# Optimization experiments

Hardware: AMD Instinct MI355X
Metric: run time of the kernel (lower is better)

The kernel has to match this reference:

```python
import jax, jax.numpy as jnp
import numpy as np

K_TOP = 4          # self.k
NUM_EXPERTS = 16   # self.num_experts
LOSS_COEF = 0.01


def setup_inputs() -> dict:
    key = jax.random.key(0)
    k0, k1, k2, k3, k4 = jax.random.split(key, 5)
    B, Cin, Cout, H, Wd, E = 16, 64, 64, 64, 64, NUM_EXPERTS
    x = jax.random.normal(k0, (B, Cin, H, Wd), dtype=jnp.float32)
    w_gate = jax.random.normal(k1, (Cin, E), dtype=jnp.float32) * 0.1
    w_noise = jax.random.normal(k2, (Cin, E), dtype=jnp.float32) * 0.1
    W = jax.random.normal(k3, (E, Cout, Cin, 3, 3), dtype=jnp.float32) * (1.0 / np.sqrt(Cin * 9).astype(np.float32))
    b = jax.random.normal(k4, (E, Cout), dtype=jnp.float32) * 0.01
    return {"x": x, "w_gate": w_gate, "w_noise": w_noise, "W": W, "b": b, "train": 0}


def _cv_squared(v):
    # torch .var() is unbiased (ddof=1)
    v = v.astype(jnp.float32)
    return jnp.var(v, ddof=1) / (jnp.mean(v) ** 2 + 1e-10)


def reference(x, w_gate, w_noise, W, b, train):
    B = x.shape[0]
    E = NUM_EXPERTS
    # gate_x = flatten(avgpool(x)) -> [B, Cin]
    gate_x = jnp.mean(x, axis=(2, 3))
    clean_logits = gate_x @ w_gate                      # [B, E]
    # train == 0 (eval): no noise branch; logits = softmax(clean_logits)
    logits = jax.nn.softmax(clean_logits, axis=1)
    top_vals, top_idx = jax.lax.top_k(logits, min(K_TOP + 1, E))
    tk_vals = top_vals[:, :K_TOP]                       # [B, k]
    tk_idx = top_idx[:, :K_TOP]                         # [B, k]
    tk_gates = tk_vals / (jnp.sum(tk_vals, axis=1, keepdims=True) + 1e-6)
    gates = jnp.zeros_like(logits).at[jnp.arange(B)[:, None], tk_idx].set(tk_gates)  # [B, E]
    # load (eval path): count of nonzero gates per expert
    load = jax.lax.stop_gradient(jnp.sum(gates > 0, axis=0)).astype(jnp.float32)     # [E]
    importance = jnp.sum(gates, axis=0)                 # [E]
    loss = (_cv_squared(importance) + _cv_squared(load)) * LOSS_COEF
    # dispatch/combine == dense gated mixture: zero-gate experts contribute 0.
    def conv_one(w):
        return jax.lax.conv_general_dilated(
            x, w, window_strides=(1, 1), padding=[(1, 1), (1, 1)],
            dimension_numbers=("NCHW", "OIHW", "NCHW"))
    expert_outs = jax.vmap(conv_one)(W) + b[:, None, :, None, None]  # [E, B, Cout, H, W]
    y = jnp.einsum("ebchw,be->bchw", expert_outs, gates)
    return (y, loss)
```

## Files before the change

kernel.cpp:

```cpp
#include <hip/hip_runtime.h>
#include <hip/hip_bf16.h>


typedef __attribute__((ext_vector_type(8))) short bf16x8;
typedef __attribute__((ext_vector_type(4))) float f32x4;

__device__ inline unsigned short f2bf(float f) {
  unsigned u = __builtin_bit_cast(unsigned, f);
  unsigned r = u + 0x7FFFu + ((u >> 16) & 1u);
  return (unsigned short)(r >> 16);
}

__global__ __launch_bounds__(256) void gatex_kernel(const float* __restrict__ x,
                                                    float* __restrict__ gate_x) {
  int bc = blockIdx.x;
  const float4* xp = (const float4*)(x + (size_t)bc * 4096);
  int t = threadIdx.x;
  float s = 0.f;
#pragma unroll
  for (int i = 0; i < 4; ++i) {
    float4 v = xp[t + i * 256];
    s += v.x + v.y + v.z + v.w;
  }
  for (int off = 32; off > 0; off >>= 1) s += __shfl_down(s, off, 64);
  __shared__ float wsum[4];
  int wid = t >> 6, lane = t & 63;
  if (lane == 0) wsum[wid] = s;
  __syncthreads();
  if (t == 0) gate_x[bc] = (wsum[0] + wsum[1] + wsum[2] + wsum[3]) * (1.0f / 4096.0f);
}

__global__ __launch_bounds__(256) void gate_kernel(const float* __restrict__ gate_x,
                                                   const float* __restrict__ w_gate,
                                                   float* __restrict__ tkg,
                                                   int* __restrict__ tki,
                                                   float* __restrict__ loss_out) {
  __shared__ float sl[16][16];
  __shared__ float sg[16][16];
  __shared__ float simp[16], sld[16];
  int t = threadIdx.x;
  int b = t >> 4, e = t & 15;
  float acc = 0.f;
  for (int c = 0; c < 64; ++c) acc += gate_x[b * 64 + c] * w_gate[c * 16 + e];
  sl[b][e] = acc;
  __syncthreads();
  if (t < 16) {
    int bb = t;
    float m = sl[bb][0];
#pragma unroll
    for (int i = 1; i < 16; ++i) m = fmaxf(m, sl[bb][i]);
    float p[16];
    float z = 0.f;
#pragma unroll
    for (int i = 0; i < 16; ++i) { p[i] = expf(sl[bb][i] - m); z += p[i]; }
#pragma unroll
    for (int i = 0; i < 16; ++i) p[i] /= z;
    int idx[4]; float val[4];
    bool used[16];
#pragma unroll
    for (int i = 0; i < 16; ++i) used[i] = false;
    for (int j = 0; j < 4; ++j) {
      int bi = 0; float bv = -1.f;
      for (int i = 0; i < 16; ++i)
        if (!used[i] && p[i] > bv) { bv = p[i]; bi = i; }
      used[bi] = true; idx[j] = bi; val[j] = bv;
    }
    float ssum = val[0] + val[1] + val[2] + val[3] + 1e-6f;
#pragma unroll
    for (int i = 0; i < 16; ++i) sg[bb][i] = 0.f;
    for (int j = 0; j < 4; ++j) {
      float g = val[j] / ssum;
      sg[bb][idx[j]] = g;
      tkg[bb * 4 + j] = g;
      tki[bb * 4 + j] = idx[j];
    }
  }
  __syncthreads();
  if (t < 16) {
    int ee = t; float imp = 0.f, ld = 0.f;
    for (int bb = 0; bb < 16; ++bb) {
      float g = sg[bb][ee];
      imp += g;
      if (g > 0.f) ld += 1.f;
    }
    simp[ee] = imp; sld[ee] = ld;
  }
  __syncthreads();
  if (t == 0) {
    float mi = 0.f, ml = 0.f;
    for (int i = 0; i < 16; ++i) { mi += simp[i]; ml += sld[i]; }
    mi *= (1.f / 16.f); ml *= (1.f / 16.f);
    float vi = 0.f, vl = 0.f;
    for (int i = 0; i < 16; ++i) {
      float d = simp[i] - mi; vi += d * d;
      float dl = sld[i] - ml; vl += dl * dl;
    }
    vi *= (1.f / 15.f); vl *= (1.f / 15.f);
    loss_out[0] = (vi / (mi * mi + 1e-10f) + vl / (ml * ml + 1e-10f)) * 0.01f;
  }
}

__global__ __launch_bounds__(256) void combine_kernel(const float* __restrict__ W,
                                                      const float* __restrict__ bias,
                                                      const float* __restrict__ tkg,
                                                      const int* __restrict__ tki,
                                                      unsigned short* __restrict__ wc,
                                                      float* __restrict__ bc) {
  int cg = blockIdx.x;
  int b = blockIdx.y;
  int t = threadIdx.x;
  __shared__ float g[4];
  __shared__ int e[4];
  if (t < 4) { g[t] = tkg[b * 4 + t]; e[t] = tki[b * 4 + t]; }
  __syncthreads();
  float g0 = g[0], g1 = g[1], g2 = g[2], g3 = g[3];
  int e0 = e[0], e1 = e[1], e2 = e[2], e3 = e[3];
  if (cg == 0 && t < 64)
    bc[b * 64 + t] = g0 * bias[e0 * 64 + t] + g1 * bias[e1 * 64 + t] +
                     g2 * bias[e2 * 64 + t] + g3 * bias[e3 * 64 + t];
  for (int idx = t; idx < 2304; idx += 256) {
    int col = idx / 576;
    int rem = idx - col * 576;
    int p = rem >> 6;
    int ci = rem & 63;
    int co = cg * 4 + col;
    int wi = (co * 64 + ci) * 9 + p;
    float v = g0 * W[e0 * 36864 + wi] + g1 * W[e1 * 36864 + wi] +
              g2 * W[e2 * 36864 + wi] + g3 * W[e3 * 36864 + wi];
    wc[((b * 64 + co) * 9 + p) * 64 + ci] = f2bf(v);
  }
}

__global__ __launch_bounds__(256) void transpose_kernel(const float* __restrict__ x,
                                                        unsigned short* __restrict__ xt) {
  int bh = blockIdx.x;
  int b = bh >> 6, h = bh & 63;
  __shared__ float tile[64][65];
  int t = threadIdx.x;
  int w = t & 63, c0 = t >> 6;
#pragma unroll
  for (int i = 0; i < 16; ++i) {
    int ci = c0 * 16 + i;
    tile[ci][w] = x[(((size_t)b * 64 + ci) * 64 + h) * 64 + w];
  }
  __syncthreads();
#pragma unroll
  for (int it = 0; it < 2; ++it) {
    int idx = t + it * 256;
    int wo = idx >> 3;
    int cgi = (idx & 7) * 8;
    bf16x8 v;
#pragma unroll
    for (int j = 0; j < 8; ++j)
      v[j] = (short)f2bf(tile[cgi + j][wo]);
    *(bf16x8*)(xt + ((((size_t)b * 64 + h) * 64 + wo) * 64 + cgi)) = v;
  }
}

__global__ __launch_bounds__(256) void conv_mfma(const unsigned short* __restrict__ xt,
                                                 const unsigned short* __restrict__ wc,
                                                 const float* __restrict__ bc,
                                                 float* __restrict__ y) {
  int rt = blockIdx.x;
  int b = blockIdx.y;
  int tid = threadIdx.x;
  int wv = tid >> 6, L = tid & 63;
  int lane15 = L & 15, quad = L >> 4;
  int row = rt * 2 + (wv >> 1);
  int colbase = (wv & 1) * 32;
  const unsigned short* xtb = xt + ((size_t)b << 18);
  const unsigned short* wcb = wc + (size_t)b * 36864;
  f32x4 acc[4][2];
#pragma unroll
  for (int mt = 0; mt < 4; ++mt)
#pragma unroll
    for (int nt = 0; nt < 2; ++nt) acc[mt][nt] = (f32x4){0.f, 0.f, 0.f, 0.f};
  const bf16x8 zero = {0, 0, 0, 0, 0, 0, 0, 0};
#pragma unroll
  for (int p = 0; p < 9; ++p) {
    int dr = p / 3, dc = p % 3;
    int h = row + dr - 1;
    bool hok = (unsigned)h < 64u;
#pragma unroll
    for (int ck = 0; ck < 2; ++ck) {
      int kb = ck * 32 + quad * 8;
      bf16x8 bf[2];
#pragma unroll
      for (int nt = 0; nt < 2; ++nt) {
        int w = colbase + nt * 16 + lane15 + dc - 1;
        bf16x8 v = zero;
        if (hok && (unsigned)w < 64u)
          v = *(const bf16x8*)(xtb + (((h << 6) + w) << 6) + kb);
        bf[nt] = v;
      }
      bf16x8 af[4];
#pragma unroll
      for (int mt = 0; mt < 4; ++mt) {
        int co = mt * 16 + lane15;
        af[mt] = *(const bf16x8*)(wcb + (co * 9 + p) * 64 + kb);
      }
#pragma unroll
      for (int mt = 0; mt < 4; ++mt)
#pragma unroll
        for (int nt = 0; nt < 2; ++nt)
          acc[mt][nt] = __builtin_amdgcn_mfma_f32_16x16x32_bf16(af[mt], bf[nt], acc[mt][nt], 0, 0, 0);
    }
  }
#pragma unroll
  for (int mt = 0; mt < 4; ++mt) {
#pragma unroll
    for (int r = 0; r < 4; ++r) {
      int co = mt * 16 + quad * 4 + r;
      float bias = bc[(b << 6) + co];
#pragma unroll
      for (int nt = 0; nt < 2; ++nt) {
        int w = colbase + nt * 16 + lane15;
        y[(((size_t)(b << 6) + co) << 12) + (row << 6) + w] = acc[mt][nt][r] + bias;
      }
    }
  }
}

extern "C" void kernel_launch(void* const* d_in, const int* in_sizes, int n_in,
                              void* d_out, int out_size, void* d_ws, size_t ws_size,
                              hipStream_t stream) {
  const float* x = (const float*)d_in[0];
  const float* w_gate = (const float*)d_in[1];
  const float* W = (const float*)d_in[3];
  const float* bias = (const float*)d_in[4];
  float* out = (float*)d_out;
  float* ws = (float*)d_ws;

  float* gate_x = ws;
  float* tkg = ws + 1024;
  int* tki = (int*)(ws + 1088);
  float* bc = ws + 1152;
  unsigned short* wc = (unsigned short*)(ws + 2176);
  unsigned short* xt = (unsigned short*)(ws + 297088);

  gatex_kernel<<<1024, 256, 0, stream>>>(x, gate_x);
  transpose_kernel<<<1024, 256, 0, stream>>>(x, xt);
  gate_kernel<<<1, 256, 0, stream>>>(gate_x, w_gate, tkg, tki, out + 4194304);
  {
    dim3 grid(16, 16);
    combine_kernel<<<grid, 256, 0, stream>>>(W, bias, tkg, tki, wc, bc);
  }
  {
    dim3 grid(32, 16);
    conv_mfma<<<grid, 256, 0, stream>>>(xt, wc, bc, out);
  }
}
```

Before: 124.0 us.

## Fuse gate pooling into transpose, re-layout operands, widen conv tile per wave

Folds the per-channel mean pooling into the transpose kernel through per-row partial sums, which removes the separate pass that read all of x a second time. The gate kernel then reduces those partials. Activations and combined weights move to a channel-group-of-8 blocked layout so MFMA fragment loads are contiguous. Each conv wave now computes a full 64-wide row (4x4 accumulators), which halves the grid and increases reuse of weight fragments. The cost is that the combine kernel drops to 16 blocks, so less parallelism is available for the weight mixing.

Measured after the change: 180.0 us. 45.2% more time.

```diff
diff --git a/kernel.cpp b/kernel.cpp
--- a/kernel.cpp
+++ b/kernel.cpp
@@ -11,38 +11,63 @@
   return (unsigned short)(r >> 16);
 }
 
-__global__ __launch_bounds__(256) void gatex_kernel(const float* __restrict__ x,
-                                                    float* __restrict__ gate_x) {
-  int bc = blockIdx.x;
-  const float4* xp = (const float4*)(x + (size_t)bc * 4096);
+__global__ __launch_bounds__(256) void transpose_kernel(const float* __restrict__ x,
+                                                        unsigned short* __restrict__ xt,
+                                                        float* __restrict__ gpart) {
+  int bh = blockIdx.x;
+  int b = bh >> 6, h = bh & 63;
+  __shared__ float tile[64][65];
   int t = threadIdx.x;
-  float s = 0.f;
-#pragma unroll
-  for (int i = 0; i < 4; ++i) {
-    float4 v = xp[t + i * 256];
-    s += v.x + v.y + v.z + v.w;
-  }
-  for (int off = 32; off > 0; off >>= 1) s += __shfl_down(s, off, 64);
-  __shared__ float wsum[4];
-  int wid = t >> 6, lane = t & 63;
-  if (lane == 0) wsum[wid] = s;
-  __syncthreads();
-  if (t == 0) gate_x[bc] = (wsum[0] + wsum[1] + wsum[2] + wsum[3]) * (1.0f / 4096.0f);
-}
-
-__global__ __launch_bounds__(256) void gate_kernel(const float* __restrict__ gate_x,
+  int w = t & 63, c0 = t >> 6;
+#pragma unroll
+  for (int i = 0; i < 16; ++i) {
+    int ci = c0 * 16 + i;
+    tile[ci][w] = x[(((size_t)b * 64 + ci) * 64 + h) * 64 + w];
+  }
+  __syncthreads();
+  if (t < 64) {
+    float s = 0.f;
+#pragma unroll
+    for (int w2 = 0; w2 < 64; ++w2) s += tile[t][w2];
+    gpart[(size_t)bh * 64 + t] = s;
+  }
+#pragma unroll
+  for (int it = 0; it < 2; ++it) {
+    int idx = t + it * 256;
+    int g = idx >> 6;
+    int wo = idx & 63;
+    bf16x8 v;
+#pragma unroll
+    for (int j = 0; j < 8; ++j) v[j] = (short)f2bf(tile[g * 8 + j][wo]);
+    *(bf16x8*)(xt + (((size_t)bh * 8 + g) * 64 + wo) * 8) = v;
+  }
+}
+
+__global__ __launch_bounds__(256) void gate_kernel(const float* __restrict__ gpart,
                                                    const float* __restrict__ w_gate,
                                                    float* __restrict__ tkg,
                                                    int* __restrict__ tki,
                                                    float* __restrict__ loss_out) {
+  __shared__ float sgx[16][64];
   __shared__ float sl[16][16];
   __shared__ float sg[16][16];
   __shared__ float simp[16], sld[16];
   int t = threadIdx.x;
-  int b = t >> 4, e = t & 15;
-  float acc = 0.f;
-  for (int c = 0; c < 64; ++c) acc += gate_x[b * 64 + c] * w_gate[c * 16 + e];
-  sl[b][e] = acc;
+#pragma unroll
+  for (int k = 0; k < 4; ++k) {
+    int pi = t + k * 256;
+    int b = pi >> 6, ci = pi & 63;
+    float s = 0.f;
+    for (int h = 0; h < 64; ++h) s += gpart[((size_t)b * 64 + h) * 64 + ci];
+    sgx[b][ci] = s * (1.0f / 4096.0f);
+  }
+  __syncthreads();
+  {
+    int b = t >> 4, e = t & 15;
+    float acc = 0.f;
+    for (int c = 0; c < 64; ++c) acc += sgx[b][c] * w_gate[c * 16 + e];
+    sl[b][e] = acc;
+  }
   __syncthreads();
   if (t < 16) {
     int bb = t;
@@ -106,8 +131,7 @@
                                                       const int* __restrict__ tki,
                                                       unsigned short* __restrict__ wc,
                                                       float* __restrict__ bc) {
-  int cg = blockIdx.x;
-  int b = blockIdx.y;
+  int b = blockIdx.x;
   int t = threadIdx.x;
   __shared__ float g[4];
   __shared__ int e[4];
@@ -115,45 +139,24 @@
   __syncthreads();
   float g0 = g[0], g1 = g[1], g2 = g[2], g3 = g[3];
   int e0 = e[0], e1 = e[1], e2 = e[2], e3 = e[3];
-  if (cg == 0 && t < 64)
+  if (t < 64)
     bc[b * 64 + t] = g0 * bias[e0 * 64 + t] + g1 * bias[e1 * 64 + t] +
                      g2 * bias[e2 * 64 + t] + g3 * bias[e3 * 64 + t];
-  for (int idx = t; idx < 2304; idx += 256) {
-    int col = idx / 576;
-    int rem = idx - col * 576;
-    int p = rem >> 6;
-    int ci = rem & 63;
-    int co = cg * 4 + col;
-    int wi = (co * 64 + ci) * 9 + p;
-    float v = g0 * W[e0 * 36864 + wi] + g1 * W[e1 * 36864 + wi] +
-              g2 * W[e2 * 36864 + wi] + g3 * W[e3 * 36864 + wi];
-    wc[((b * 64 + co) * 9 + p) * 64 + ci] = f2bf(v);
-  }
-}
-
-__global__ __launch_bounds__(256) void transpose_kernel(const float* __restrict__ x,
-                                                        unsigned short* __restrict__ xt) {
-  int bh = blockIdx.x;
-  int b = bh >> 6, h = bh & 63;
-  __shared__ float tile[64][65];
-  int t = threadIdx.x;
-  int w = t & 63, c0 = t >> 6;
-#pragma unroll
-  for (int i = 0; i < 16; ++i) {
-    int ci = c0 * 16 + i;
-    tile[ci][w] = x[(((size_t)b * 64 + ci) * 64 + h) * 64 + w];
-  }
-  __syncthreads();
-#pragma unroll
-  for (int it = 0; it < 2; ++it) {
-    int idx = t + it * 256;
-    int wo = idx >> 3;
-    int cgi = (idx & 7) * 8;
+  for (int idx = t; idx < 4608; idx += 256) {
+    int e8 = idx * 8;
+    int p = e8 >> 12;
+    int gg = (e8 >> 9) & 7;
+    int co = (e8 >> 3) & 63;
     bf16x8 v;
 #pragma unroll
-    for (int j = 0; j < 8; ++j)
-      v[j] = (short)f2bf(tile[cgi + j][wo]);
-    *(bf16x8*)(xt + ((((size_t)b * 64 + h) * 64 + wo) * 64 + cgi)) = v;
+    for (int j = 0; j < 8; ++j) {
+      int ci = gg * 8 + j;
+      int wi = (co * 64 + ci) * 9 + p;
+      float f = g0 * W[e0 * 36864 + wi] + g1 * W[e1 * 36864 + wi] +
+                g2 * W[e2 * 36864 + wi] + g3 * W[e3 * 36864 + wi];
+      v[j] = (short)f2bf(f);
+    }
+    *(bf16x8*)(wc + (size_t)b * 36864 + e8) = v;
   }
 }
 
@@ -166,15 +169,14 @@
   int tid = threadIdx.x;
   int wv = tid >> 6, L = tid & 63;
   int lane15 = L & 15, quad = L >> 4;
-  int row = rt * 2 + (wv >> 1);
-  int colbase = (wv & 1) * 32;
+  int row = rt * 4 + wv;
   const unsigned short* xtb = xt + ((size_t)b << 18);
   const unsigned short* wcb = wc + (size_t)b * 36864;
-  f32x4 acc[4][2];
+  f32x4 acc[4][4];
 #pragma unroll
   for (int mt = 0; mt < 4; ++mt)
 #pragma unroll
-    for (int nt = 0; nt < 2; ++nt) acc[mt][nt] = (f32x4){0.f, 0.f, 0.f, 0.f};
+    for (int nt = 0; nt < 4; ++nt) acc[mt][nt] = (f32x4){0.f, 0.f, 0.f, 0.f};
   const bf16x8 zero = {0, 0, 0, 0, 0, 0, 0, 0};
 #pragma unroll
   for (int p = 0; p < 9; ++p) {
@@ -183,27 +185,25 @@
     bool hok = (unsigned)h < 64u;
 #pragma unroll
     for (int ck = 0; ck < 2; ++ck) {
-      int kb = ck * 32 + quad * 8;
-      bf16x8 bf[2];
-#pragma unroll
-      for (int nt = 0; nt < 2; ++nt) {
-        int w = colbase + nt * 16 + lane15 + dc - 1;
+      int g = ck * 4 + quad;
+      bf16x8 bfr[4];
+#pragma unroll
+      for (int nt = 0; nt < 4; ++nt) {
+        int w = nt * 16 + lane15 + dc - 1;
         bf16x8 v = zero;
         if (hok && (unsigned)w < 64u)
-          v = *(const bf16x8*)(xtb + (((h << 6) + w) << 6) + kb);
-        bf[nt] = v;
+          v = *(const bf16x8*)(xtb + (((h << 3) + g) << 9) + (w << 3));
+        bfr[nt] = v;
       }
-      bf16x8 af[4];
-#pragma unroll
-      for (int mt = 0; mt < 4; ++mt) {
-        int co = mt * 16 + lane15;
-        af[mt] = *(const bf16x8*)(wcb + (co * 9 + p) * 64 + kb);
-      }
+      bf16x8 afr[4];
 #pragma unroll
       for (int mt = 0; mt < 4; ++mt)
-#pragma unroll
-        for (int nt = 0; nt < 2; ++nt)
-          acc[mt][nt] = __builtin_amdgcn_mfma_f32_16x16x32_bf16(af[mt], bf[nt], acc[mt][nt], 0, 0, 0);
+        afr[mt] = *(const bf16x8*)(wcb + ((((p << 3) + g) << 6) + mt * 16 + lane15) * 8);
+#pragma unroll
+      for (int mt = 0; mt < 4; ++mt)
+#pragma unroll
+        for (int nt = 0; nt < 4; ++nt)
+          acc[mt][nt] = __builtin_amdgcn_mfma_f32_16x16x32_bf16(afr[mt], bfr[nt], acc[mt][nt], 0, 0, 0);
     }
   }
 #pragma unroll
@@ -213,8 +213,8 @@
       int co = mt * 16 + quad * 4 + r;
       float bias = bc[(b << 6) + co];
 #pragma unroll
-      for (int nt = 0; nt < 2; ++nt) {
-        int w = colbase + nt * 16 + lane15;
+      for (int nt = 0; nt < 4; ++nt) {
+        int w = nt * 16 + lane15;
         y[(((size_t)(b << 6) + co) << 12) + (row << 6) + w] = acc[mt][nt][r] + bias;
       }
     }
@@ -231,22 +231,18 @@
   float* out = (float*)d_out;
   float* ws = (float*)d_ws;
 
-  float* gate_x = ws;
-  float* tkg = ws + 1024;
-  int* tki = (int*)(ws + 1088);
-  float* bc = ws + 1152;
-  unsigned short* wc = (unsigned short*)(ws + 2176);
-  unsigned short* xt = (unsigned short*)(ws + 297088);
-
-  gatex_kernel<<<1024, 256, 0, stream>>>(x, gate_x);
-  transpose_kernel<<<1024, 256, 0, stream>>>(x, xt);
-  gate_kernel<<<1, 256, 0, stream>>>(gate_x, w_gate, tkg, tki, out + 4194304);
+  float* gpart = ws;
+  float* tkg = ws + 65536;
+  int* tki = (int*)(ws + 65600);
+  float* bc = ws + 65664;
+  unsigned short* wc = (unsigned short*)(ws + 66688);
+  unsigned short* xt = (unsigned short*)(ws + 361600);
+
+  transpose_kernel<<<1024, 256, 0, stream>>>(x, xt, gpart);
+  gate_kernel<<<1, 256, 0, stream>>>(gpart, w_gate, tkg, tki, out + 4194304);
+  combine_kernel<<<16, 256, 0, stream>>>(W, bias, tkg, tki, wc, bc);
   {
     dim3 grid(16, 16);
-    combine_kernel<<<grid, 256, 0, stream>>>(W, bias, tkg, tki, wc, bc);
-  }
-  {
-    dim3 grid(32, 16);
     conv_mfma<<<grid, 256, 0, stream>>>(xt, wc, bc, out);
   }
 }
```
